# Kernel tuning notes

Measured on AMD Instinct MI355X. Metric: run time of the kernel, lower is better.

## Reference

```python
import jax, jax.numpy as jnp
import numpy as np


def conv1x1(x, W, b=None):
    # 1x1 conv == channel matmul: x (B,C,H,W), W (O,C)
    y = jnp.einsum('oc,bchw->bohw', W, x)
    if b is not None:
        y = y + b[None, :, None, None]
    return y


def setup_inputs() -> dict:
    key = jax.random.key(0)
    ks = jax.random.split(key, 20)
    B, C_l, C_h, H, W, d = 2, 64, 192, 64, 64, 128
    s = 0.02
    return {
        'll': jax.random.normal(ks[0], (B, C_l, H, W), jnp.float32),
        'hf': jax.random.normal(ks[1], (B, C_h, H, W), jnp.float32),
        'Wqh': jax.random.normal(ks[2], (d, C_h), jnp.float32) * s,
        'Wkh': jax.random.normal(ks[3], (d, C_h), jnp.float32) * s,
        'Wvh': jax.random.normal(ks[4], (d, C_h), jnp.float32) * s,
        'Wql': jax.random.normal(ks[5], (d, C_l), jnp.float32) * s,
        'Wkl': jax.random.normal(ks[6], (d, C_l), jnp.float32) * s,
        'Wvl': jax.random.normal(ks[7], (d, C_l), jnp.float32) * s,
        'Wph': jax.random.normal(ks[8], (C_h, d), jnp.float32) * s,
        'bph': jnp.zeros((C_h,), jnp.float32),
        'Wpl': jax.random.normal(ks[9], (C_l, d), jnp.float32) * s,
        'bpl': jnp.zeros((C_l,), jnp.float32),
        'Wah': jax.random.normal(ks[10], (C_h, C_h), jnp.float32) * s,
        'bah': jnp.zeros((C_h,), jnp.float32),
        'Wal': jax.random.normal(ks[11], (C_l, C_l), jnp.float32) * s,
        'bal': jnp.zeros((C_l,), jnp.float32),
        'alpha': jnp.ones((4,), jnp.float32),
    }


def reference(ll, hf, Wqh, Wkh, Wvh, Wql, Wkl, Wvl, Wph, bph, Wpl, bpl,
              Wah, bah, Wal, bal, alpha):
    B, C_l, H, W = ll.shape
    d = Wqh.shape[0]
    N = H * W
    scl = d ** (-0.5)

    Qh = conv1x1(hf, Wqh).reshape(B, d, N)
    Kh = conv1x1(hf, Wkh).reshape(B, d, N)
    Vh = conv1x1(hf, Wvh).reshape(B, d, N)
    Ql = conv1x1(ll, Wql).reshape(B, d, N)
    Kl = conv1x1(ll, Wkl).reshape(B, d, N)
    Vl = conv1x1(ll, Wvl).reshape(B, d, N)

    wdir = jax.nn.softmax(alpha)  # [row, col, diag, global]

    def sdpa(q, k, v):  # q,k,v: (B, L, d)
        a = jax.nn.softmax(jnp.einsum('bqd,bkd->bqk', q, k) * scl, axis=-1)
        return jnp.einsum('bqk,bkd->bqd', a, v)

    # ---- global: full N x N cross attention ----
    OL = sdpa(Qh.transpose(0, 2, 1), Kl.transpose(0, 2, 1), Vl.transpose(0, 2, 1)).transpose(0, 2, 1)
    OH = sdpa(Ql.transpose(0, 2, 1), Kh.transpose(0, 2, 1), Vh.transpose(0, 2, 1)).transpose(0, 2, 1)
    out_ll = conv1x1(OL.reshape(B, d, H, W), Wpl, bpl) * wdir[3]
    out_hf = conv1x1(OH.reshape(B, d, H, W), Wph, bph) * wdir[3]

    # ---- axial (row / col) attention ----
    def axial(q, k, v, row):
        perm = (0, 2, 3, 1) if row else (0, 3, 2, 1)  # (B,S,L,d)
        qr = q.reshape(B, d, H, W).transpose(perm)
        kr = k.reshape(B, d, H, W).transpose(perm)
        vr = v.reshape(B, d, H, W).transpose(perm)
        a = jax.nn.softmax(jnp.einsum('bsqd,bskd->bsqk', qr, kr) * scl, axis=-1)
        o = jnp.einsum('bsqk,bskd->bsqd', a, vr)
        inv = (0, 3, 1, 2) if row else (0, 3, 2, 1)
        return o.transpose(inv)  # (B,d,H,W)

    out_ll = out_ll + conv1x1(axial(Qh, Kl, Vl, True), Wpl, bpl) * wdir[0]
    out_hf = out_hf + conv1x1(axial(Ql, Kh, Vh, True), Wph, bph) * wdir[0]
    out_ll = out_ll + conv1x1(axial(Qh, Kl, Vl, False), Wpl, bpl) * wdir[1]
    out_hf = out_hf + conv1x1(axial(Ql, Kh, Vh, False), Wph, bph) * wdir[1]

    # ---- diag: faithful to original code (gather by diag index, attend, scatter back) ----
    i = jnp.arange(H)[:, None]
    j = jnp.arange(W)[None, :]
    flat_idx = (j - i + (H - 1)).reshape(-1)  # (N,), values in [0, H+W-2]

    def dsel(x):  # (B,d,N) -> (B,N,d) gathered along position axis
        return x[:, :, flat_idx].transpose(0, 2, 1)

    Ld = sdpa(dsel(Qh), dsel(Kl), dsel(Vl)).transpose(0, 2, 1)  # (B,d,N)
    Hd = sdpa(dsel(Ql), dsel(Kh), dsel(Vh)).transpose(0, 2, 1)
    blank_l = jnp.zeros((B, d, N), Ld.dtype).at[:, :, flat_idx].set(Ld)
    blank_h = jnp.zeros((B, d, N), Hd.dtype).at[:, :, flat_idx].set(Hd)
    out_ll = out_ll + conv1x1(blank_l.reshape(B, d, H, W), Wpl, bpl) * wdir[2]
    out_hf = out_hf + conv1x1(blank_h.reshape(B, d, H, W), Wph, bph) * wdir[2]

    ll_out = conv1x1(ll + out_ll, Wal, bal)
    hf_out = conv1x1(hf + out_hf, Wah, bah)
    return (ll_out, hf_out)
```

## Files before the change

### kernel.cpp

```cpp
#include <hip/hip_runtime.h>
#include <math.h>

#define N_  4096
#define D_  128
#define B_  2
#define CL_ 64
#define CH_ 192

typedef __attribute__((ext_vector_type(8))) short short8;
typedef __attribute__((ext_vector_type(4))) float f32x4;
typedef __attribute__((ext_vector_type(16))) float f32x16;

#if __has_builtin(__builtin_amdgcn_exp2f)
#define EXP2(x) __builtin_amdgcn_exp2f(x)
#else
#define EXP2(x) exp2f(x)
#endif

__device__ __forceinline__ short f2bf(float x) {
  union { float f; unsigned u; } v; v.f = x;
  unsigned r = v.u + 0x7FFFu + ((v.u >> 16) & 1u);
  return (short)(r >> 16);
}

typedef __attribute__((address_space(1))) const void gv_t;
typedef __attribute__((address_space(3))) void sv_t;
__device__ __forceinline__ void gl_lds16(const void* g, void* l) {
  __builtin_amdgcn_global_load_lds((gv_t*)g, (sv_t*)l, 16, 0, 0);
}

#define CVTPK(d, lo, hi) asm("v_cvt_pk_bf16_f32 %0, %1, %2" : "=v"(d) : "v"(lo), "v"(hi))
#define PLSWAP(a, b) asm("v_permlane32_swap_b32 %0, %1" : "+v"(a), "+v"(b))

__global__ __launch_bounds__(256)
void vt_kernel(const short* __restrict__ Vhb, const short* __restrict__ Vlb,
               short* __restrict__ Vht, short* __restrict__ Vlt) {
  __shared__ short rowbuf[4 * 4096];
  const int tid = threadIdx.x;
  const int lane = tid & 63, w = tid >> 6;
  const short* src = blockIdx.y ? Vlb : Vhb;
  short* dst = blockIdx.y ? Vlt : Vht;
  const int r0 = blockIdx.x * 4;
  #pragma unroll
  for (int i = 0; i < 8; ++i) {
    int idx = i * 256 + w * 64 + lane;
    int row = idx >> 9, g = idx & 511;
    gl_lds16(src + (size_t)(r0 + row) * N_ + g * 8,
             (char*)rowbuf + i * 4096 + w * 1024 + lane * 16);
  }
  __syncthreads();
  const int rw = r0 + w, d7 = rw & 7;
  const short* rb = rowbuf + w * 4096;
  const int w0 = (lane & 7) * 8, h0 = (lane >> 3) * 8;
  short8 rr[8];
  #pragma unroll
  for (int j = 0; j < 8; ++j)
    rr[j] = *(const short8*)(rb + (h0 + j) * 64 + (((w0 >> 3) ^ d7) * 8));
  #pragma unroll
  for (int i = 0; i < 8; ++i) {
    short8 o;
    #pragma unroll
    for (int j = 0; j < 8; ++j) o[j] = rr[j][i];
    *(short8*)(dst + (size_t)rw * N_ + (w0 + i) * 64 + (((h0 >> 3) ^ d7) * 8)) = o;
  }
}

struct QkvP {
  const float *W0h, *W1h, *W2h, *W0l, *W1l, *W2l;
  const float *Xh, *Xl;
  short *QbH, *KbH, *VbH, *QtH, *KtH;
  short *QbL, *KbL, *VbL, *QtL, *KtL;
  float qscale;
};

__global__ __launch_bounds__(256, 2)
void qkv_kernel(QkvP g) {
  __shared__ __align__(16) char BT[24576];
  __shared__ __align__(16) char AS[8192];
  __shared__ __align__(16) float Ls[64][67];
  const int tid = threadIdx.x;
  const int lane = tid & 63, w = tid >> 6, m = lane & 15, hi = lane >> 4;
  const int n0 = blockIdx.x * 64;
  const int sel = blockIdx.y >> 1, dhalf = blockIdx.y & 1, ot0 = dhalf * 64;
  const int b = blockIdx.z >> 1, s = blockIdx.z & 1;
  const int C = s ? CL_ : CH_;
  const float* Wm = s ? (sel == 0 ? g.W0l : sel == 1 ? g.W1l : g.W2l)
                      : (sel == 0 ? g.W0h : sel == 1 ? g.W1h : g.W2h);
  const float* Xs = (s ? g.Xl : g.Xh) + (size_t)b * C * N_;
  const int C2 = C * 2;

  for (int cc = 0; cc < C; cc += 64) {
    #pragma unroll
    for (int r = 0; r < 16; ++r) {
      int flat = r * 256 + tid;
      int c = flat >> 6, nn = flat & 63;
      Ls[c][nn] = Xs[(size_t)(cc + c) * N_ + n0 + nn];
    }
    __syncthreads();
    #pragma unroll
    for (int e = 0; e < 2; ++e) {
      int u = e * 256 + tid;
      int nn = u >> 3, gl = u & 7;
      short8 v;
      #pragma unroll
      for (int j = 0; j < 8; ++j) v[j] = f2bf(Ls[gl*8 + j][nn]);
      int pos = (gl ^ (nn & 7)) & 7;
      *(short8*)(BT + nn * C2 + cc * 2 + pos * 16) = v;
    }
    __syncthreads();
  }

  f32x4 acc[4];
  #pragma unroll
  for (int i = 0; i < 4; ++i) acc[i] = (f32x4){0.f, 0.f, 0.f, 0.f};

  for (int c0 = 0; c0 < C; c0 += 64) {
    __syncthreads();
    {
      int o = tid >> 2, cq = tid & 3;
      const float* wp = Wm + (size_t)(ot0 + o) * C + c0 + cq * 16;
      float4 fa = *(const float4*)(wp + 0);
      float4 fb = *(const float4*)(wp + 4);
      float4 fc = *(const float4*)(wp + 8);
      float4 fd = *(const float4*)(wp + 12);
      short8 v0 = { f2bf(fa.x), f2bf(fa.y), f2bf(fa.z), f2bf(fa.w),
                    f2bf(fb.x), f2bf(fb.y), f2bf(fb.z), f2bf(fb.w) };
      short8 v1 = { f2bf(fc.x), f2bf(fc.y), f2bf(fc.z), f2bf(fc.w),
                    f2bf(fd.x), f2bf(fd.y), f2bf(fd.z), f2bf(fd.w) };
      int g0 = cq * 2;
      *(short8*)(AS + o * 128 + (((g0) ^ (o & 7)) * 16)) = v0;
      *(short8*)(AS + o * 128 + (((g0 + 1) ^ (o & 7)) * 16)) = v1;
    }
    __syncthreads();
    const int orow = w * 16 + m;
    short8 a0 = *(const short8*)(AS + orow * 128 + (((hi) ^ (orow & 7)) * 16));
    short8 a1 = *(const short8*)(AS + orow * 128 + (((4 + hi) ^ (orow & 7)) * 16));
    #pragma unroll
    for (int nf = 0; nf < 4; ++nf) {
      int nrow = nf * 16 + m;
      const char* brow = BT + nrow * C2 + c0 * 2;
      short8 b0 = *(const short8*)(brow + (((hi) ^ (nrow & 7)) * 16));
      short8 b1 = *(const short8*)(brow + (((4 + hi) ^ (nrow & 7)) * 16));
      acc[nf] = __builtin_amdgcn_mfma_f32_16x16x32_bf16(a0, b0, acc[nf], 0, 0, 0);
      acc[nf] = __builtin_amdgcn_mfma_f32_16x16x32_bf16(a1, b1, acc[nf], 0, 0, 0);
    }
  }

  __syncthreads();
  #pragma unroll
  for (int nf = 0; nf < 4; ++nf)
    #pragma unroll
    for (int r = 0; r < 4; ++r)
      Ls[w * 16 + hi * 4 + r][nf * 16 + m] = acc[nf][r];
  __syncthreads();

  if (sel < 2) {
    float sc = (sel == 0) ? g.qscale : 1.f;
    short* QK = (sel == 0 ? (s ? g.QbL : g.QbH) : (s ? g.KbL : g.KbH)) + (size_t)b * N_ * D_;
    short* QKt = (sel == 0 ? (s ? g.QtL : g.QtH) : (s ? g.KtL : g.KtH)) + (size_t)b * N_ * D_;
    const int bx = blockIdx.x;
    #pragma unroll
    for (int e = 0; e < 2; ++e) {
      int u = tid + 256 * e;
      int nn = u >> 3, gl = u & 7;
      short8 v;
      #pragma unroll
      for (int j = 0; j < 8; ++j) v[j] = f2bf(Ls[gl*8 + j][nn] * sc);
      int posb = (dhalf * 8) | ((gl ^ (nn & 7)) & 7);
      *(short8*)(QK + (size_t)(n0 + nn) * D_ + posb * 8) = v;
      int post = (dhalf * 8) | ((gl ^ (bx & 7)) & 7);
      *(short8*)(QKt + (size_t)(nn * 64 + bx) * D_ + post * 8) = v;
    }
  } else {
    short* Vb = (s ? g.VbL : g.VbH) + (size_t)b * D_ * N_;
    #pragma unroll
    for (int e = 0; e < 2; ++e) {
      int u = tid + 256 * e;
      int o = u >> 3, gl = u & 7;
      int d = ot0 + o;
      short8 v;
      #pragma unroll
      for (int j = 0; j < 8; ++j) v[j] = f2bf(Ls[o][gl*8 + j]);
      *(short8*)(Vb + (size_t)d * N_ + n0 + ((gl ^ (d & 7)) * 8)) = v;
    }
  }
}

struct SmP {
  const short *Qhb, *Qlb, *Khb, *Klb, *Vhb, *Vlb;
  const short *Qht, *Qlt, *Kht, *Klt, *Vht, *Vlt;
  float *Mrl, *Mrh, *Mcl, *Mch, *Mdl, *Mdh;
  const float* alpha;
};

__global__ __launch_bounds__(256, 2)
void attn_sm(SmP p) {
  __shared__ __align__(16) char smem[49152];
  const int tid = threadIdx.x;
  const int lane = tid & 63, w = tid >> 6, m = lane & 15, hi = lane >> 4;

  const int bxg = blockIdx.x;
  int variant, y, bz, qx;
  if (bxg < 256)      { variant = 0; y = bxg & 63;        bz = bxg >> 6;        qx = 0; }
  else if (bxg < 512) { variant = 1; y = (bxg-256) & 63;  bz = (bxg-256) >> 6;  qx = 0; }
  else                { variant = 2; y = 0;               bz = (bxg-512) >> 1;  qx = (bxg-512) & 1; }
  const int b = bz >> 1, pair = bz & 1;
  const int widx = variant;
  const int cwflag = (variant == 2);
  const int qbase = (variant == 2) ? qx * 64 : y * 64;
  const int kcol0 = (variant == 2) ? 0 : y * 64;
  const int Lk = (variant == 2) ? 127 : 64;
  const int lqloc = (variant == 2) ? (qx ? 63 : 64) : 64;

  const short *Qs, *Ks, *Vs;
  if (variant == 1) {
    Qs = pair ? p.Qlt : p.Qht; Ks = pair ? p.Kht : p.Klt; Vs = pair ? p.Vht : p.Vlt;
  } else {
    Qs = pair ? p.Qlb : p.Qhb; Ks = pair ? p.Khb : p.Klb; Vs = pair ? p.Vhb : p.Vlb;
  }
  Qs += (size_t)b * N_ * D_; Ks += (size_t)b * N_ * D_; Vs += (size_t)b * D_ * N_;
  float* Mout;
  if (variant == 0)      Mout = (pair ? p.Mrh : p.Mrl) + (size_t)b * D_ * N_;
  else if (variant == 1) Mout = (pair ? p.Mch : p.Mcl) + (size_t)b * D_ * N_;
  else                   Mout = (pair ? p.Mdh : p.Mdl) + (size_t)b * D_ * 128;

  float a0 = p.alpha[0], a1 = p.alpha[1], a2 = p.alpha[2], a3 = p.alpha[3];
  float am = fmaxf(fmaxf(a0, a1), fmaxf(a2, a3));
  float e0 = __expf(a0-am), e1 = __expf(a1-am), e2 = __expf(a2-am), e3 = __expf(a3-am);
  float wsel = (widx == 0 ? e0 : widx == 1 ? e1 : e2) / (e0 + e1 + e2 + e3);

  auto stageK = [&](int kt) {
    #pragma unroll
    for (int i = 0; i < 4; ++i) {
      int chunk = w * 4 + i;
      gl_lds16(Ks + (size_t)(kcol0 + kt*64) * D_ + chunk * 512 + lane * 8,
               smem + 16384 + chunk * 1024);
    }
  };
  auto stageV = [&](int kt) {
    #pragma unroll
    for (int i = 0; i < 4; ++i) {
      int chunk = w * 4 + i;
      gl_lds16(Vs + (size_t)(chunk*8 + (lane>>3)) * N_ + kcol0 + kt*64 + (lane&7)*8,
               smem + 32768 + chunk * 1024);
    }
  };
  #pragma unroll
  for (int i = 0; i < 4; ++i) {
    int chunk = w * 4 + i;
    gl_lds16(Qs + (size_t)qbase * D_ + chunk * 512 + lane * 8, smem + chunk * 1024);
  }
  stageK(0); stageV(0);
  __syncthreads();

  const int qrow = w * 16 + m;
  short8 qf[4];
  #pragma unroll
  for (int cs = 0; cs < 4; ++cs)
    qf[cs] = *(const short8*)(smem + qrow * 256 + ((cs*64 + hi*16) ^ ((qrow & 7) << 4)));
  __syncthreads();

  f32x4 oacc[8];
  #pragma unroll
  for (int i = 0; i < 8; ++i) oacc[i] = (f32x4){0.f, 0.f, 0.f, 0.f};
  float m_run[4] = {-INFINITY, -INFINITY, -INFINITY, -INFINITY};
  float l_run[4] = {0.f, 0.f, 0.f, 0.f};
  char* const pstrip = smem + w * 2048;
  const int NT = (Lk + 63) >> 6;

  for (int kt = 0; kt < NT; ++kt) {
    const char* Kc = smem + 16384;
    const char* Vc = smem + 32768;
    f32x4 sacc[4];
    #pragma unroll
    for (int kf = 0; kf < 4; ++kf) sacc[kf] = (f32x4){0.f, 0.f, 0.f, 0.f};
    #pragma unroll
    for (int kf = 0; kf < 4; ++kf) {
      const int krow = kf * 16 + m;
      const char* kr = Kc + krow * 256;
      #pragma unroll
      for (int cs = 0; cs < 4; ++cs) {
        short8 kfr = *(const short8*)(kr + ((cs*64 + hi*16) ^ ((krow & 7) << 4)));
        sacc[kf] = __builtin_amdgcn_mfma_f32_16x16x32_bf16(qf[cs], kfr, sacc[kf], 0, 0, 0);
      }
    }
    float cw[4];
    #pragma unroll
    for (int kf = 0; kf < 4; ++kf) {
      if (cwflag) {
        int kg = kt * 64 + kf * 16 + m;
        int dd = kg - 63; dd = dd < 0 ? -dd : dd;
        cw[kf] = (kg < Lk) ? (float)(64 - dd) : 0.f;
      } else cw[kf] = 1.f;
    }
    #pragma unroll
    for (int r = 0; r < 4; ++r) {
      float mt = fmaxf(fmaxf(sacc[0][r], sacc[1][r]), fmaxf(sacc[2][r], sacc[3][r]));
      mt = fmaxf(mt, __shfl_xor(mt, 1));
      mt = fmaxf(mt, __shfl_xor(mt, 2));
      mt = fmaxf(mt, __shfl_xor(mt, 4));
      mt = fmaxf(mt, __shfl_xor(mt, 8));
      float mn = fmaxf(m_run[r], mt);
      float corr = EXP2(m_run[r] - mn);
      m_run[r] = mn;
      const int rl = hi * 4 + r;
      char* prow = pstrip + rl * 128;
      float psum = 0.f;
      #pragma unroll
      for (int kf = 0; kf < 4; ++kf) {
        float pv = cw[kf] * EXP2(sacc[kf][r] - mn);
        psum += pv;
        int kcol = (kf * 16 + m) * 2;
        *(short*)(prow + (kcol ^ ((rl & 7) << 4))) = f2bf(pv);
      }
      psum += __shfl_xor(psum, 1);
      psum += __shfl_xor(psum, 2);
      psum += __shfl_xor(psum, 4);
      psum += __shfl_xor(psum, 8);
      l_run[r] = l_run[r] * corr + psum;
      #pragma unroll
      for (int cf = 0; cf < 8; ++cf) oacc[cf][r] *= corr;
    }
    #pragma unroll
    for (int ks = 0; ks < 2; ++ks) {
      short8 pa = *(const short8*)(pstrip + m * 128 + ((ks*64 + hi*16) ^ ((m & 7) << 4)));
      #pragma unroll
      for (int cf = 0; cf < 8; ++cf) {
        const int crow = cf * 16 + m;
        short8 vf = *(const short8*)(Vc + crow * 128 + ((ks*64 + hi*16) ^ ((crow & 7) << 4)));
        oacc[cf] = __builtin_amdgcn_mfma_f32_16x16x32_bf16(pa, vf, oacc[cf], 0, 0, 0);
      }
    }
    __syncthreads();
    if (kt + 1 < NT) { stageK(kt + 1); stageV(kt + 1); __syncthreads(); }
  }

  float inv[4];
  #pragma unroll
  for (int r = 0; r < 4; ++r) inv[r] = wsel / l_run[r];
  float* Os = (float*)smem;
  #pragma unroll
  for (int cf = 0; cf < 8; ++cf)
    #pragma unroll
    for (int r = 0; r < 4; ++r)
      Os[(cf*16 + m) * 66 + w * 16 + hi * 4 + r] = oacc[cf][r] * inv[r];
  __syncthreads();
  for (int it = 0; it < 32; ++it) {
    int flat = it * 256 + tid;
    int c = flat >> 6, qq = flat & 63;
    if (qq < lqloc) {
      float v = Os[c * 66 + qq];
      if (variant == 0)      Mout[(size_t)c * N_ + qbase + qq] = v;
      else if (variant == 1) Mout[(size_t)c * N_ + qq * 64 + y] = v;
      else                   Mout[c * 128 + qbase + qq] = v;
    }
  }
}

#define GVQ 65536

struct GlobalAttnParams {
  const short *Qhb, *Qlb, *Khb, *Klb, *Vhb, *Vlb;
  const float *Mrl, *Mrh, *Mcl, *Mch, *Mdl, *Mdh;
  short *Mtbl, *Mtbh;
  const float* alpha;
};

__global__ __launch_bounds__(512, 1)
void attn_gl_kernel(GlobalAttnParams p) {
  __shared__ __align__(16) char smem[131072];
  const int tid = threadIdx.x;
  const int lane = tid & 63, w = tid >> 6;
  const int wid = w & 1, gsel = w >> 1;
  const int key = lane & 31, kh = lane >> 5;

  const int bx = blockIdx.x;
  const int xcd = bx & 7, sub = bx >> 3;
  const int pz = xcd >> 1;
  const int b = pz >> 1, pair = pz & 1;
  const int q0 = ((xcd & 1) * 32 + sub) * 64;

  const short* Qb = (pair ? p.Qlb : p.Qhb) + (size_t)b * N_ * D_;
  const short* Kb = (pair ? p.Khb : p.Klb) + (size_t)b * N_ * D_;
  const short* Vb = (pair ? p.Vhb : p.Vlb) + (size_t)b * D_ * N_;
  const float* Mr = (pair ? p.Mrh : p.Mrl) + (size_t)b * D_ * N_;
  const float* Mc = (pair ? p.Mch : p.Mcl) + (size_t)b * D_ * N_;
  const float* Md = (pair ? p.Mdh : p.Mdl) + (size_t)b * D_ * 128;
  short* Mtb = (pair ? p.Mtbh : p.Mtbl) + (size_t)b * N_ * D_;

  float a0 = p.alpha[0], a1 = p.alpha[1], a2 = p.alpha[2], a3 = p.alpha[3];
  float am = fmaxf(fmaxf(a0,a1), fmaxf(a2,a3));
  float e0 = __expf(a0-am), e1 = __expf(a1-am), e2 = __expf(a2-am), e3 = __expf(a3-am);
  const float wsel = e3 / (e0+e1+e2+e3);

  auto stageQuad = [&](int qd) {
    #pragma unroll
    for (int i = 0; i < 8; ++i) {
      int c = w*8 + i;
      if (c < 32) {
        int tk = c >> 3, ck = c & 7;
        gl_lds16(Kb + (size_t)((4*qd + tk)*32 + ck*4)*D_ + lane*8,
                 smem + (qd & 1)*32768 + tk*8192 + ck*1024);
      } else {
        int cc = c - 32;
        int d = cc*4 + (lane >> 4);
        int g = lane & 15, kb2 = g >> 3, gg = g & 7;
        gl_lds16(Vb + (size_t)d*N_ + qd*128 + kb2*64 + ((gg ^ (d & 7))*8),
                 smem + GVQ + (qd & 1)*32768 + cc*1024);
      }
    }
  };

  const int qq = wid*32 + key;
  const short* qrow_g = Qb + (size_t)(q0 + qq) * D_;
  short8 qf[8];
  #pragma unroll
  for (int fi = 0; fi < 8; ++fi)
    qf[fi] = *(const short8*)(qrow_g + (((fi*2 + kh) ^ (qq & 7)) << 3));

  stageQuad(0);

  f32x16 oacc[4];
  #pragma unroll
  for (int d = 0; d < 4; ++d)
    #pragma unroll
    for (int r = 0; r < 16; ++r) oacc[d][r] = 0.f;
  float m_run = -INFINITY, l_run = 0.f;

  const int NQ = N_ / 128;
  for (int j = 0; j < NQ; ++j) {
    __syncthreads();
    if (j + 1 < NQ) stageQuad(j + 1);

    const char* Kc = smem + (j & 1)*32768 + gsel*8192;
    const char* Vc = smem + GVQ + (j & 1)*32768;

    f32x16 sacc;
    #pragma unroll
    for (int r = 0; r < 16; ++r) sacc[r] = 0.f;
    __builtin_amdgcn_s_setprio(1);
    #pragma unroll
    for (int fi = 0; fi < 8; ++fi) {
      short8 kf = *(const short8*)(Kc + key*256 + (((fi*2 + kh) ^ (key & 7)) << 4));
      sacc = __builtin_amdgcn_mfma_f32_32x32x16_bf16(kf, qf[fi], sacc, 0, 0, 0);
    }
    __builtin_amdgcn_s_setprio(0);

    float mt = sacc[0];
    #pragma unroll
    for (int r = 1; r < 16; ++r) mt = fmaxf(mt, sacc[r]);
    { float aa = mt, bb = mt; PLSWAP(aa, bb); mt = fmaxf(aa, bb); }
    if (!__all(mt <= m_run + 8.f)) {
      float mn = fmaxf(m_run, mt);
      float corr = EXP2(m_run - mn);
      m_run = mn;
      l_run *= corr;
      #pragma unroll
      for (int d = 0; d < 4; ++d)
        #pragma unroll
        for (int r = 0; r < 16; ++r) oacc[d][r] *= corr;
    }
    float pv[16];
    float psum = 0.f;
    #pragma unroll
    for (int r = 0; r < 16; ++r) { pv[r] = EXP2(sacc[r] - m_run); psum += pv[r]; }
    { float sa = psum, sb = psum; PLSWAP(sa, sb); psum = sa + sb; }
    l_run += psum;

    union U8 { unsigned u[4]; short8 s; } pf0, pf1;
    {
      unsigned c0, c1, c2, c3;
      CVTPK(c0, pv[0], pv[1]);  CVTPK(c1, pv[2], pv[3]);
      CVTPK(c2, pv[4], pv[5]);  CVTPK(c3, pv[6], pv[7]);
      PLSWAP(c0, c2); PLSWAP(c1, c3);
      pf0.u[0] = c0; pf0.u[1] = c1; pf0.u[2] = c2; pf0.u[3] = c3;
      CVTPK(c0, pv[8],  pv[9]);  CVTPK(c1, pv[10], pv[11]);
      CVTPK(c2, pv[12], pv[13]); CVTPK(c3, pv[14], pv[15]);
      PLSWAP(c0, c2); PLSWAP(c1, c3);
      pf1.u[0] = c0; pf1.u[1] = c1; pf1.u[2] = c2; pf1.u[3] = c3;
    }

    __builtin_amdgcn_s_setprio(1);
    #pragma unroll
    for (int d = 0; d < 4; ++d) {
      #pragma unroll
      for (int ks = 0; ks < 2; ++ks) {
        int crow = d*32 + key;
        int gidx = gsel*4 + ks*2 + kh;
        int kb2 = gidx >> 3, gg = gidx & 7;
        short8 vf = *(const short8*)(Vc + crow*256 + kb2*128 + ((gg ^ (key & 7)) << 4));
        oacc[d] = __builtin_amdgcn_mfma_f32_32x32x16_bf16(vf, (ks ? pf1.s : pf0.s), oacc[d], 0, 0, 0);
      }
    }
    __builtin_amdgcn_s_setprio(0);
  }
  __syncthreads();

  float* MLbase = (float*)(smem + 98304);
  if (gsel > 0) {
    int idx = (gsel - 1)*2 + wid;
    float* ob = (float*)smem + idx*4096;
    #pragma unroll
    for (int d = 0; d < 4; ++d)
      #pragma unroll
      for (int r = 0; r < 16; ++r)
        ob[(d*16 + r)*64 + lane] = oacc[d][r];
    float* ml = MLbase + idx*128;
    ml[lane] = m_run;
    ml[64 + lane] = l_run;
  }
  __syncthreads();

  float inv = 0.f;
  if (gsel == 0) {
    float mp[3], lp[3];
    float mn = m_run;
    #pragma unroll
    for (int pi = 0; pi < 3; ++pi) {
      const float* ml = MLbase + (pi*2 + wid)*128;
      mp[pi] = ml[lane]; lp[pi] = ml[64 + lane];
      mn = fmaxf(mn, mp[pi]);
    }
    float cA = EXP2(m_run - mn);
    float lt = l_run * cA;
    #pragma unroll
    for (int d = 0; d < 4; ++d)
      #pragma unroll
      for (int r = 0; r < 16; ++r) oacc[d][r] *= cA;
    #pragma unroll
    for (int pi = 0; pi < 3; ++pi) {
      float cp = EXP2(mp[pi] - mn);
      lt += lp[pi] * cp;
      const float* ob = (const float*)smem + (pi*2 + wid)*4096;
      #pragma unroll
      for (int d = 0; d < 4; ++d)
        #pragma unroll
        for (int r = 0; r < 16; ++r)
          oacc[d][r] += ob[(d*16 + r)*64 + lane] * cp;
    }
    inv = wsel / lt;
  }
  __syncthreads();

  float* Os = (float*)smem;
  if (gsel == 0) {
    #pragma unroll
    for (int d = 0; d < 4; ++d)
      #pragma unroll
      for (int r = 0; r < 16; ++r) {
        int dr = d*32 + (r & 3) + 8*(r >> 2) + 4*kh;
        Os[dr*66 + qq] = oacc[d][r] * inv;
      }
  }
  __syncthreads();

  for (int it = 0; it < 16; ++it) {
    int flat = it*512 + tid;
    int c = flat >> 6, q2 = flat & 63;
    int pos = q0 + q2;
    float add = Mr[(size_t)c*N_ + pos] + Mc[(size_t)c*N_ + pos];
    if (pos < 127) add += Md[c*128 + pos];
    Os[c*66 + q2] += add;
  }
  __syncthreads();
  #pragma unroll
  for (int e = 0; e < 2; ++e) {
    int u = tid + 512*e;
    int nn = u >> 4, gb = u & 15;
    short8 v;
    #pragma unroll
    for (int jj = 0; jj < 8; ++jj) v[jj] = f2bf(Os[(gb*8 + jj)*66 + nn]);
    int pos = (gb & 8) | ((gb ^ (nn & 7)) & 7);
    *(short8*)(Mtb + (size_t)(q0 + nn)*D_ + pos*8) = v;
  }
}

struct Gemm2P {
  const float *WA; const short *BA; const float *resA, *biasA; float *outA; short *UtA; int KA, OA;
  const float *WB; const short *BB; const float *resB, *biasB; float *outB; short *UtB; int KB, OB;
  int ysplit, epmode;
};

__global__ __launch_bounds__(256, 4)
void gemm2_bf16(Gemm2P g) {
  __shared__ __align__(16) char AB[16384];
  __shared__ float Epi[64][67];
  const int tid = threadIdx.x;
  const int lane = tid & 63, w = tid >> 6, m = lane & 15, hi = lane >> 4;
  const int n0 = blockIdx.x * 64;
  const int b = blockIdx.z;
  const int yy = blockIdx.y;
  const bool isB = yy >= g.ysplit;
  const int ot0 = (isB ? (yy - g.ysplit) : yy) * 64;
  const float* Wm = isB ? g.WB : g.WA;
  const int K = isB ? g.KB : g.KA;
  const int O = isB ? g.OB : g.OA;
  const short* Bs = (isB ? g.BB : g.BA) + (size_t)b * N_ * K;

  f32x4 acc[4];
  #pragma unroll
  for (int i = 0; i < 4; ++i) acc[i] = (f32x4){0.f, 0.f, 0.f, 0.f};

  for (int c0 = 0; c0 < K; c0 += 64) {
    __syncthreads();
    {
      int o = tid >> 2, cq = tid & 3;
      const float* wp = Wm + (size_t)(ot0 + o) * K + c0 + cq * 16;
      float4 fa = *(const float4*)(wp + 0);
      float4 fb = *(const float4*)(wp + 4);
      float4 fc = *(const float4*)(wp + 8);
      float4 fd = *(const float4*)(wp + 12);
      short8 v0 = { f2bf(fa.x), f2bf(fa.y), f2bf(fa.z), f2bf(fa.w),
                    f2bf(fb.x), f2bf(fb.y), f2bf(fb.z), f2bf(fb.w) };
      short8 v1 = { f2bf(fc.x), f2bf(fc.y), f2bf(fc.z), f2bf(fc.w),
                    f2bf(fd.x), f2bf(fd.y), f2bf(fd.z), f2bf(fd.w) };
      int g0 = cq * 2;
      *(short8*)(AB + o * 128 + (((g0) ^ (o & 7)) * 16)) = v0;
      *(short8*)(AB + o * 128 + (((g0 + 1) ^ (o & 7)) * 16)) = v1;
    }
    #pragma unroll
    for (int e = 0; e < 2; ++e) {
      int cid = e * 256 + w * 64 + lane;
      int nn = cid >> 3, gs = cid & 7;
      gl_lds16(Bs + (size_t)(n0 + nn) * K + c0 + gs * 8,
               AB + 8192 + e * 4096 + w * 1024 + lane * 16);
    }
    __syncthreads();
    const int orow = w * 16 + m;
    short8 a0 = *(const short8*)(AB + orow * 128 + (((hi) ^ (orow & 7)) * 16));
    short8 a1 = *(const short8*)(AB + orow * 128 + (((4 + hi) ^ (orow & 7)) * 16));
    #pragma unroll
    for (int nf = 0; nf < 4; ++nf) {
      int nrow = nf * 16 + m;
      short8 b0 = *(const short8*)(AB + 8192 + nrow * 128 + (((hi) ^ (nrow & 7)) * 16));
      short8 b1 = *(const short8*)(AB + 8192 + nrow * 128 + (((4 + hi) ^ (nrow & 7)) * 16));
      acc[nf] = __builtin_amdgcn_mfma_f32_16x16x32_bf16(a0, b0, acc[nf], 0, 0, 0);
      acc[nf] = __builtin_amdgcn_mfma_f32_16x16x32_bf16(a1, b1, acc[nf], 0, 0, 0);
    }
  }

  #pragma unroll
  for (int nf = 0; nf < 4; ++nf)
    #pragma unroll
    for (int r = 0; r < 4; ++r)
      Epi[w * 16 + hi * 4 + r][nf * 16 + m] = acc[nf][r];
  __syncthreads();

  if (g.epmode == 1) {
    const float* res = (isB ? g.resB : g.resA) + (size_t)b * O * N_;
    const float* bias = isB ? g.biasB : g.biasA;
    short* Ut = (isB ? g.UtB : g.UtA) + (size_t)b * N_ * O;
    #pragma unroll
    for (int e = 0; e < 2; ++e) {
      int nn = tid & 63;
      int gl = (tid >> 6) + e * 4;
      int ob = ot0 + gl * 8;
      short8 v;
      #pragma unroll
      for (int j = 0; j < 8; ++j)
        v[j] = f2bf(Epi[gl*8 + j][nn] + res[(size_t)(ob + j) * N_ + n0 + nn] + bias[ob + j]);
      int gout = (ot0 >> 3) + gl;
      int pos = (gout & ~7) | ((gout ^ (nn & 7)) & 7);
      *(short8*)(Ut + (size_t)(n0 + nn) * O + pos * 8) = v;
    }
  } else {
    const float* bias = isB ? g.biasB : g.biasA;
    float* outF = isB ? g.outB : g.outA;
    int o = tid >> 2, nq = tid & 3;
    float bv = bias[ot0 + o];
    float* dst = outF + (size_t)b * O * N_ + (size_t)(ot0 + o) * N_ + n0 + nq * 16;
    #pragma unroll
    for (int q4 = 0; q4 < 4; ++q4) {
      float4 vv = { Epi[o][nq*16 + q4*4 + 0] + bv, Epi[o][nq*16 + q4*4 + 1] + bv,
                    Epi[o][nq*16 + q4*4 + 2] + bv, Epi[o][nq*16 + q4*4 + 3] + bv };
      *(float4*)(dst + q4 * 4) = vv;
    }
  }
}

extern "C" void kernel_launch(void* const* d_in, const int* in_sizes, int n_in,
                              void* d_out, int out_size, void* d_ws, size_t ws_size,
                              hipStream_t stream) {
  (void)in_sizes; (void)n_in; (void)out_size; (void)ws_size;
  const float* ll  = (const float*)d_in[0];
  const float* hf  = (const float*)d_in[1];
  const float* Wqh = (const float*)d_in[2];
  const float* Wkh = (const float*)d_in[3];
  const float* Wvh = (const float*)d_in[4];
  const float* Wql = (const float*)d_in[5];
  const float* Wkl = (const float*)d_in[6];
  const float* Wvl = (const float*)d_in[7];
  const float* Wph = (const float*)d_in[8];
  const float* bph = (const float*)d_in[9];
  const float* Wpl = (const float*)d_in[10];
  const float* bpl = (const float*)d_in[11];
  const float* Wah = (const float*)d_in[12];
  const float* bah = (const float*)d_in[13];
  const float* Wal = (const float*)d_in[14];
  const float* bal = (const float*)d_in[15];
  const float* alpha = (const float*)d_in[16];

  float* ws = (float*)d_ws;
  const size_t BDN = (size_t)B_ * D_ * N_;
  float* Mrl = ws;
  float* Mrh = Mrl + BDN;
  float* Mcl = Mrh + BDN;
  float* Mch = Mcl + BDN;
  float* Mdl = Mch + BDN;
  float* Mdh = Mdl + (size_t)B_ * D_ * 128;
  short* sp = (short*)(Mdh + (size_t)B_ * D_ * 128);
  short* Qhb = sp;           sp += BDN;
  short* Qlb = sp;           sp += BDN;
  short* Khb = sp;           sp += BDN;
  short* Klb = sp;           sp += BDN;
  short* Vhb = sp;           sp += BDN;
  short* Vlb = sp;           sp += BDN;
  short* Qht = sp;           sp += BDN;
  short* Qlt = sp;           sp += BDN;
  short* Kht = sp;           sp += BDN;
  short* Klt = sp;           sp += BDN;
  short* Vht = sp;           sp += BDN;
  short* Vlt = sp;           sp += BDN;
  short* Mtbl = Qht;
  short* Mtbh = Qlt;
  short* Utl  = Kht;
  short* Uth  = Klt;

  dim3 blk(256, 1, 1);
  const float qscale = (float)(0.08838834764831845 * 1.4426950408889634);
  float* out = (float*)d_out;

  QkvP qp{Wqh, Wkh, Wvh, Wql, Wkl, Wvl, hf, ll,
          Qhb, Khb, Vhb, Qht, Kht, Qlb, Klb, Vlb, Qlt, Klt, qscale};
  qkv_kernel<<<dim3(N_/64, 6, 2*B_), blk, 0, stream>>>(qp);

  vt_kernel<<<dim3(64, 2), blk, 0, stream>>>(Vhb, Vlb, Vht, Vlt);

  SmP smp{Qhb, Qlb, Khb, Klb, Vhb, Vlb, Qht, Qlt, Kht, Klt, Vht, Vlt,
          Mrl, Mrh, Mcl, Mch, Mdl, Mdh, alpha};
  attn_sm<<<dim3(520, 1, 1), blk, 0, stream>>>(smp);

  GlobalAttnParams gp{Qhb, Qlb, Khb, Klb, Vhb, Vlb,
                      Mrl, Mrh, Mcl, Mch, Mdl, Mdh, Mtbl, Mtbh, alpha};
  attn_gl_kernel<<<dim3(256, 1, 1), dim3(512,1,1), 0, stream>>>(gp);

  Gemm2P wp{Wpl, Mtbl, ll, bpl, nullptr, Utl, D_, CL_,
            Wph, Mtbh, hf, bph, nullptr, Uth, D_, CH_, 1, 1};
  gemm2_bf16<<<dim3(N_/64, 4, B_), blk, 0, stream>>>(wp);

  Gemm2P wa{Wal, Utl, nullptr, bal, out, nullptr, CL_, CL_,
            Wah, Uth, nullptr, bah, out + (size_t)B_*CL_*N_, nullptr, CH_, CH_, 1, 2};
  gemm2_bf16<<<dim3(N_/64, 4, B_), blk, 0, stream>>>(wa);
}
```

Measured before the change: 119.3 us.

## Fold projection weights into final conv and split QK MFMA accumulation chains

Precomputes Wa·Wp and the combined bias in a small weight-prep kernel. The two back-to-back output GEMMs become one GEMM over the concatenated [attention output; input] with K = D + C, so the intermediate bf16 buffer round trip and one kernel launch go away. qkv_kernel now also writes a bf16 position-major copy of the inputs for that GEMM. Separately, the QK^T MFMA chain in global attention is split into two independent accumulators to shorten the dependency chain. The trade-off is extra writes of the transposed inputs, a second kernel launch for weight prep, and extra adds to merge the two accumulators.

```diff
diff --git a/kernel.cpp b/kernel.cpp
--- a/kernel.cpp
+++ b/kernel.cpp
@@ -31,6 +31,66 @@
 
 #define CVTPK(d, lo, hi) asm("v_cvt_pk_bf16_f32 %0, %1, %2" : "=v"(d) : "v"(lo), "v"(hi))
 #define PLSWAP(a, b) asm("v_permlane32_swap_b32 %0, %1" : "+v"(a), "+v"(b))
+
+struct WprepP {
+  const float *WaL, *WpL, *bpL, *baL;
+  const float *WaH, *WpH, *bpH, *baH;
+  float *WapL, *bapL, *WapH, *bapH;
+};
+
+__global__ __launch_bounds__(256)
+void wprep_kernel(WprepP g) {
+  __shared__ float Wt[32][68];
+  __shared__ float Xt[32][68];
+  const int tid = threadIdx.x;
+  const int tx = tid & 15, ty = tid >> 4;
+  const int d0 = blockIdx.x * 64;
+  const float *Wa, *Wp, *bp, *ba; float *Wap, *bap; int C, o0;
+  if (blockIdx.y == 0) { Wa=g.WaL; Wp=g.WpL; bp=g.bpL; ba=g.baL; Wap=g.WapL; bap=g.bapL; C=CL_; o0=0; }
+  else { Wa=g.WaH; Wp=g.WpH; bp=g.bpH; ba=g.baH; Wap=g.WapH; bap=g.bapH; C=CH_; o0=(blockIdx.y-1)*64; }
+
+  float acc[4][4];
+  #pragma unroll
+  for (int i = 0; i < 4; ++i)
+    #pragma unroll
+    for (int j = 0; j < 4; ++j) acc[i][j] = 0.f;
+
+  for (int c0 = 0; c0 < C; c0 += 32) {
+    __syncthreads();
+    #pragma unroll
+    for (int r = 0; r < 8; ++r) {
+      int flat = r*256 + tid;
+      int oo = flat >> 5, c = flat & 31;
+      Wt[c][oo] = Wa[(size_t)(o0 + oo)*C + c0 + c];
+    }
+    #pragma unroll
+    for (int r = 0; r < 8; ++r) {
+      int flat = r*256 + tid;
+      int c = flat >> 6, dd = flat & 63;
+      Xt[c][dd] = Wp[(size_t)(c0 + c)*D_ + d0 + dd];
+    }
+    __syncthreads();
+    #pragma unroll 8
+    for (int c = 0; c < 32; ++c) {
+      float4 wv = *(const float4*)&Wt[c][ty << 2];
+      float4 xv = *(const float4*)&Xt[c][tx << 2];
+      acc[0][0] += wv.x*xv.x; acc[0][1] += wv.x*xv.y; acc[0][2] += wv.x*xv.z; acc[0][3] += wv.x*xv.w;
+      acc[1][0] += wv.y*xv.x; acc[1][1] += wv.y*xv.y; acc[1][2] += wv.y*xv.z; acc[1][3] += wv.y*xv.w;
+      acc[2][0] += wv.z*xv.x; acc[2][1] += wv.z*xv.y; acc[2][2] += wv.z*xv.z; acc[2][3] += wv.z*xv.w;
+      acc[3][0] += wv.w*xv.x; acc[3][1] += wv.w*xv.y; acc[3][2] += wv.w*xv.z; acc[3][3] += wv.w*xv.w;
+    }
+  }
+  #pragma unroll
+  for (int i = 0; i < 4; ++i)
+    *(float4*)&Wap[(size_t)(o0 + (ty<<2) + i)*D_ + d0 + (tx<<2)] =
+        make_float4(acc[i][0], acc[i][1], acc[i][2], acc[i][3]);
+
+  if (blockIdx.x == 0 && tid < 64) {
+    float sum = ba[o0 + tid];
+    for (int c = 0; c < C; ++c) sum += Wa[(size_t)(o0 + tid)*C + c] * bp[c];
+    bap[o0 + tid] = sum;
+  }
+}
 
 __global__ __launch_bounds__(256)
 void vt_kernel(const short* __restrict__ Vhb, const short* __restrict__ Vlb,
@@ -70,6 +130,7 @@
   const float *Xh, *Xl;
   short *QbH, *KbH, *VbH, *QtH, *KtH;
   short *QbL, *KbL, *VbL, *QtL, *KtL;
+  short *XtH, *XtL;
   float qscale;
 };
 
@@ -110,6 +171,15 @@
     __syncthreads();
   }
 
+  if (blockIdx.y == 0) {
+    short* xT = (s ? g.XtL : g.XtH) + (size_t)b * N_ * C + (size_t)n0 * C;
+    const int NG = C >> 3;
+    for (int u = tid; u < 64 * NG; u += 256) {
+      int nn = u / NG, gg = u - nn * NG;
+      *(short8*)(xT + (size_t)nn * C + gg * 8) = *(const short8*)(BT + nn * C2 + gg * 16);
+    }
+  }
+
   f32x4 acc[4];
   #pragma unroll
   for (int i = 0; i < 4; ++i) acc[i] = (f32x4){0.f, 0.f, 0.f, 0.f};
@@ -435,16 +505,20 @@
     const char* Kc = smem + (j & 1)*32768 + gsel*8192;
     const char* Vc = smem + GVQ + (j & 1)*32768;
 
-    f32x16 sacc;
-    #pragma unroll
-    for (int r = 0; r < 16; ++r) sacc[r] = 0.f;
+    f32x16 sa, sb2;
+    #pragma unroll
+    for (int r = 0; r < 16; ++r) { sa[r] = 0.f; sb2[r] = 0.f; }
     __builtin_amdgcn_s_setprio(1);
     #pragma unroll
     for (int fi = 0; fi < 8; ++fi) {
       short8 kf = *(const short8*)(Kc + key*256 + (((fi*2 + kh) ^ (key & 7)) << 4));
-      sacc = __builtin_amdgcn_mfma_f32_32x32x16_bf16(kf, qf[fi], sacc, 0, 0, 0);
+      if (fi & 1) sb2 = __builtin_amdgcn_mfma_f32_32x32x16_bf16(kf, qf[fi], sb2, 0, 0, 0);
+      else        sa  = __builtin_amdgcn_mfma_f32_32x32x16_bf16(kf, qf[fi], sa, 0, 0, 0);
     }
     __builtin_amdgcn_s_setprio(0);
+    f32x16 sacc;
+    #pragma unroll
+    for (int r = 0; r < 16; ++r) sacc[r] = sa[r] + sb2[r];
 
     float mt = sacc[0];
     #pragma unroll
@@ -464,7 +538,7 @@
     float psum = 0.f;
     #pragma unroll
     for (int r = 0; r < 16; ++r) { pv[r] = EXP2(sacc[r] - m_run); psum += pv[r]; }
-    { float sa = psum, sb = psum; PLSWAP(sa, sb); psum = sa + sb; }
+    { float sap = psum, sbp = psum; PLSWAP(sap, sbp); psum = sap + sbp; }
     l_run += psum;
 
     union U8 { unsigned u[4]; short8 s; } pf0, pf1;
@@ -575,37 +649,41 @@
   }
 }
 
-struct Gemm2P {
-  const float *WA; const short *BA; const float *resA, *biasA; float *outA; short *UtA; int KA, OA;
-  const float *WB; const short *BB; const float *resB, *biasB; float *outB; short *UtB; int KB, OB;
-  int ysplit, epmode;
+struct GfP {
+  const float *WapL, *WaL, *bapL; const short *MtbL, *XtL;
+  const float *WapH, *WaH, *bapH; const short *MtbH, *XtH;
+  float *outL, *outH;
 };
 
 __global__ __launch_bounds__(256, 4)
-void gemm2_bf16(Gemm2P g) {
+void gemm_final(GfP g) {
   __shared__ __align__(16) char AB[16384];
   __shared__ float Epi[64][67];
   const int tid = threadIdx.x;
   const int lane = tid & 63, w = tid >> 6, m = lane & 15, hi = lane >> 4;
   const int n0 = blockIdx.x * 64;
   const int b = blockIdx.z;
-  const int yy = blockIdx.y;
-  const bool isB = yy >= g.ysplit;
-  const int ot0 = (isB ? (yy - g.ysplit) : yy) * 64;
-  const float* Wm = isB ? g.WB : g.WA;
-  const int K = isB ? g.KB : g.KA;
-  const int O = isB ? g.OB : g.OA;
-  const short* Bs = (isB ? g.BB : g.BA) + (size_t)b * N_ * K;
+  const bool isH = blockIdx.y >= 1;
+  const int ot0 = (isH ? blockIdx.y - 1 : 0) * 64;
+  const int C = isH ? CH_ : CL_;
+  const int O = C;
+  const float* Wap = isH ? g.WapH : g.WapL;
+  const float* Wa  = isH ? g.WaH  : g.WaL;
+  const float* bap = isH ? g.bapH : g.bapL;
+  const short* Mtb = (isH ? g.MtbH : g.MtbL) + (size_t)b * N_ * D_;
+  const short* Xt  = (isH ? g.XtH : g.XtL) + (size_t)b * N_ * C;
+  const int Ktot = D_ + C;
 
   f32x4 acc[4];
   #pragma unroll
   for (int i = 0; i < 4; ++i) acc[i] = (f32x4){0.f, 0.f, 0.f, 0.f};
 
-  for (int c0 = 0; c0 < K; c0 += 64) {
+  for (int c0 = 0; c0 < Ktot; c0 += 64) {
     __syncthreads();
     {
       int o = tid >> 2, cq = tid & 3;
-      const float* wp = Wm + (size_t)(ot0 + o) * K + c0 + cq * 16;
+      const float* wp = (c0 < D_) ? (Wap + (size_t)(ot0 + o) * D_ + c0 + cq * 16)
+                                  : (Wa  + (size_t)(ot0 + o) * C + (c0 - D_) + cq * 16);
       float4 fa = *(const float4*)(wp + 0);
       float4 fb = *(const float4*)(wp + 4);
       float4 fc = *(const float4*)(wp + 8);
@@ -622,8 +700,9 @@
     for (int e = 0; e < 2; ++e) {
       int cid = e * 256 + w * 64 + lane;
       int nn = cid >> 3, gs = cid & 7;
-      gl_lds16(Bs + (size_t)(n0 + nn) * K + c0 + gs * 8,
-               AB + 8192 + e * 4096 + w * 1024 + lane * 16);
+      const short* src = (c0 < D_) ? (Mtb + (size_t)(n0 + nn) * D_ + c0 + gs * 8)
+                                   : (Xt  + (size_t)(n0 + nn) * C + (c0 - D_) + gs * 8);
+      gl_lds16(src, AB + 8192 + e * 4096 + w * 1024 + lane * 16);
     }
     __syncthreads();
     const int orow = w * 16 + m;
@@ -646,35 +725,15 @@
       Epi[w * 16 + hi * 4 + r][nf * 16 + m] = acc[nf][r];
   __syncthreads();
 
-  if (g.epmode == 1) {
-    const float* res = (isB ? g.resB : g.resA) + (size_t)b * O * N_;
-    const float* bias = isB ? g.biasB : g.biasA;
-    short* Ut = (isB ? g.UtB : g.UtA) + (size_t)b * N_ * O;
-    #pragma unroll
-    for (int e = 0; e < 2; ++e) {
-      int nn = tid & 63;
-      int gl = (tid >> 6) + e * 4;
-      int ob = ot0 + gl * 8;
-      short8 v;
-      #pragma unroll
-      for (int j = 0; j < 8; ++j)
-        v[j] = f2bf(Epi[gl*8 + j][nn] + res[(size_t)(ob + j) * N_ + n0 + nn] + bias[ob + j]);
-      int gout = (ot0 >> 3) + gl;
-      int pos = (gout & ~7) | ((gout ^ (nn & 7)) & 7);
-      *(short8*)(Ut + (size_t)(n0 + nn) * O + pos * 8) = v;
-    }
-  } else {
-    const float* bias = isB ? g.biasB : g.biasA;
-    float* outF = isB ? g.outB : g.outA;
-    int o = tid >> 2, nq = tid & 3;
-    float bv = bias[ot0 + o];
-    float* dst = outF + (size_t)b * O * N_ + (size_t)(ot0 + o) * N_ + n0 + nq * 16;
-    #pragma unroll
-    for (int q4 = 0; q4 < 4; ++q4) {
-      float4 vv = { Epi[o][nq*16 + q4*4 + 0] + bv, Epi[o][nq*16 + q4*4 + 1] + bv,
-                    Epi[o][nq*16 + q4*4 + 2] + bv, Epi[o][nq*16 + q4*4 + 3] + bv };
-      *(float4*)(dst + q4 * 4) = vv;
-    }
+  float* outF = (isH ? g.outH : g.outL) + (size_t)b * O * N_;
+  int o = tid >> 2, nq = tid & 3;
+  float bv = bap[ot0 + o];
+  float* dst = outF + (size_t)(ot0 + o) * N_ + n0 + nq * 16;
+  #pragma unroll
+  for (int q4 = 0; q4 < 4; ++q4) {
+    float4 vv = { Epi[o][nq*16 + q4*4 + 0] + bv, Epi[o][nq*16 + q4*4 + 1] + bv,
+                  Epi[o][nq*16 + q4*4 + 2] + bv, Epi[o][nq*16 + q4*4 + 3] + bv };
+    *(float4*)(dst + q4 * 4) = vv;
   }
 }
 
@@ -708,7 +767,11 @@
   float* Mch = Mcl + BDN;
   float* Mdl = Mch + BDN;
   float* Mdh = Mdl + (size_t)B_ * D_ * 128;
-  short* sp = (short*)(Mdh + (size_t)B_ * D_ * 128);
+  float* Wapl = Mdh + (size_t)B_ * D_ * 128;
+  float* Waph = Wapl + (size_t)CL_ * D_;
+  float* bapl = Waph + (size_t)CH_ * D_;
+  float* baph = bapl + CL_;
+  short* sp = (short*)(baph + CH_);
   short* Qhb = sp;           sp += BDN;
   short* Qlb = sp;           sp += BDN;
   short* Khb = sp;           sp += BDN;
@@ -721,17 +784,20 @@
   short* Klt = sp;           sp += BDN;
   short* Vht = sp;           sp += BDN;
   short* Vlt = sp;           sp += BDN;
+  short* XtH = sp;           sp += (size_t)B_ * N_ * CH_;
+  short* XtL = sp;           sp += (size_t)B_ * N_ * CL_;
   short* Mtbl = Qht;
   short* Mtbh = Qlt;
-  short* Utl  = Kht;
-  short* Uth  = Klt;
 
   dim3 blk(256, 1, 1);
   const float qscale = (float)(0.08838834764831845 * 1.4426950408889634);
   float* out = (float*)d_out;
 
+  WprepP wpp{Wal, Wpl, bpl, bal, Wah, Wph, bph, bah, Wapl, bapl, Waph, baph};
+  wprep_kernel<<<dim3(2, 4, 1), blk, 0, stream>>>(wpp);
+
   QkvP qp{Wqh, Wkh, Wvh, Wql, Wkl, Wvl, hf, ll,
-          Qhb, Khb, Vhb, Qht, Kht, Qlb, Klb, Vlb, Qlt, Klt, qscale};
+          Qhb, Khb, Vhb, Qht, Kht, Qlb, Klb, Vlb, Qlt, Klt, XtH, XtL, qscale};
   qkv_kernel<<<dim3(N_/64, 6, 2*B_), blk, 0, stream>>>(qp);
 
   vt_kernel<<<dim3(64, 2), blk, 0, stream>>>(Vhb, Vlb, Vht, Vlt);
@@ -744,11 +810,8 @@
                       Mrl, Mrh, Mcl, Mch, Mdl, Mdh, Mtbl, Mtbh, alpha};
   attn_gl_kernel<<<dim3(256, 1, 1), dim3(512,1,1), 0, stream>>>(gp);
 
-  Gemm2P wp{Wpl, Mtbl, ll, bpl, nullptr, Utl, D_, CL_,
-            Wph, Mtbh, hf, bph, nullptr, Uth, D_, CH_, 1, 1};
-  gemm2_bf16<<<dim3(N_/64, 4, B_), blk, 0, stream>>>(wp);
-
-  Gemm2P wa{Wal, Utl, nullptr, bal, out, nullptr, CL_, CL_,
-            Wah, Uth, nullptr, bah, out + (size_t)B_*CL_*N_, nullptr, CH_, CH_, 1, 2};
-  gemm2_bf16<<<dim3(N_/64, 4, B_), blk, 0, stream>>>(wa);
+  GfP gf{Wapl, Wal, bapl, Mtbl, XtL,
+         Waph, Wah, baph, Mtbh, XtH,
+         out, out + (size_t)B_*CL_*N_};
+  gemm_final<<<dim3(N_/64, 4, B_), blk, 0, stream>>>(gf);
 }
```

New measurement: 162.4 us. 1.36x slower.
